# Kernel tuning notes

Hardware: AMD Instinct MI355X
Metric: run time of the kernel (lower is better)

The kernel has to match this reference:

```python
import jax, jax.numpy as jnp
import numpy as np

B, S, D_MODEL = 4, 2048, 1024
N_HEADS, D_HEAD = 16, 64
HIDDEN = N_HEADS * D_HEAD
N_PRIM, RANK = 16, 256
CHUNK = 64  # matches CHUNK_SIZE in the torch module


def setup_inputs() -> dict:
    key = jax.random.key(0)
    ks = jax.random.split(key, 16)
    def n(k, shape, scale=0.02):
        return jax.random.normal(k, shape, dtype=jnp.float32) * scale
    return {
        'x': jax.random.normal(ks[0], (B, S, D_MODEL), dtype=jnp.float32),
        'q_U': n(ks[1], (N_PRIM, D_MODEL, RANK)),
        'q_V': n(ks[2], (N_PRIM, RANK, HIDDEN)),
        'k_U': n(ks[3], (N_PRIM, D_MODEL, RANK)),
        'k_V': n(ks[4], (N_PRIM, RANK, HIDDEN)),
        'v_U': n(ks[5], (N_PRIM, D_MODEL, RANK)),
        'v_V': n(ks[6], (N_PRIM, RANK, HIDDEN)),
        'q_logits': jax.random.normal(ks[7], (N_PRIM,), dtype=jnp.float32),
        'k_logits': jax.random.normal(ks[8], (N_PRIM,), dtype=jnp.float32),
        'v_logits': jax.random.normal(ks[9], (N_PRIM,), dtype=jnp.float32),
        'gate_logits': jax.random.normal(ks[10], (N_PRIM,), dtype=jnp.float32),
        'decay_w': n(ks[11], (N_HEADS, D_MODEL), 0.03),
        'decay_b': jnp.full((N_HEADS,), -2.0, dtype=jnp.float32),
        'out_gate_w': n(ks[12], (HIDDEN, D_MODEL), 0.03),
        'out_proj_w': n(ks[13], (D_MODEL, HIDDEN), 0.03),
        'rms_w': jnp.ones((HIDDEN,), dtype=jnp.float32),
        'top_k': 4,
    }


def _bank_topk_fused(x, U, V, logits, top_k):
    """Top-k fused mixture of low-rank primitives: sum_j w_j * (x @ U_j @ V_j)."""
    w = jax.nn.softmax(logits)                      # [P]
    vals, idx = jax.lax.top_k(w, top_k)             # [k], [k]
    vals = vals / jnp.sum(vals)                     # renormalize selected weights
    Us = U[idx]                                     # [k, d_in, rank]
    Vs = V[idx]                                     # [k, rank, d_out]
    h = jnp.einsum('bsd,kdr->bskr', x, Us)          # low-rank bottleneck
    return jnp.einsum('bskr,kro,k->bso', h, Vs, vals)


def _chunked_scan(q, kv, log_decay):
    """Decay-gated linear recurrence via chunked parallel scan (CHUNK=64).
    q, kv: [B,S,H,D]; log_decay: [B,S,H,1]. Returns [B,S,H,D]."""
    b, s, h, d = q.shape
    nc = s // CHUNK
    # [NC, B, C, H, *] chunked layout for lax.scan over chunks
    qc = jnp.moveaxis(q.reshape(b, nc, CHUNK, h, d), 1, 0)
    kvc = jnp.moveaxis(kv.reshape(b, nc, CHUNK, h, d), 1, 0)
    ldc = jnp.moveaxis(log_decay.reshape(b, nc, CHUNK, h, 1), 1, 0)

    def step(state, inp):
        ld, kvs, qs = inp                            # [B,C,H,1], [B,C,H,D], [B,C,H,D]
        cum = jnp.cumsum(ld, axis=1)                 # cumulative log-decay in chunk
        last = cum[:, -1:]
        kv_shifted = kvs * jnp.exp(last - cum)
        new = jnp.exp(cum - last) * jnp.cumsum(kv_shifted, axis=1)
        chunk_states = state[:, None] * jnp.exp(cum) + new   # [B,C,H,D]
        out = qs * chunk_states
        return chunk_states[:, -1], out

    state0 = jnp.zeros((b, h, d), dtype=jnp.float32)
    _, outs = jax.lax.scan(step, state0, (ldc, kvc, qc))     # [NC,B,C,H,D]
    return jnp.moveaxis(outs, 0, 1).reshape(b, s, h, d)


def reference(x, q_U, q_V, k_U, k_V, v_U, v_V,
              q_logits, k_logits, v_logits, gate_logits,
              decay_w, decay_b, out_gate_w, out_proj_w, rms_w, top_k):
    b, s, _ = x.shape
    h, d = decay_w.shape[0], q_V.shape[-1] // decay_w.shape[0]

    q = _bank_topk_fused(x, q_U, q_V, q_logits, top_k).reshape(b, s, h, d)
    k = _bank_topk_fused(x, k_U, k_V, k_logits, top_k).reshape(b, s, h, d)
    v = _bank_topk_fused(x, v_U, v_V, v_logits, top_k).reshape(b, s, h, d)
    # gate shares the V bank (gate = v_bank.forward_topk_fused with gate weights)
    gate = _bank_topk_fused(x, v_U, v_V, gate_logits, top_k).reshape(b, s, h, d)

    log_decay = -jax.nn.softplus(jnp.einsum('bsd,hd->bsh', x, decay_w) + decay_b)[..., None]  # [B,S,H,1]
    kv = jax.nn.sigmoid(gate) * k * v

    out = _chunked_scan(q, kv.astype(jnp.float32), log_decay.astype(jnp.float32))
    out = out.reshape(b, s, h * d)

    # RMSNorm (torch default eps = finfo.eps for fp32)
    eps = jnp.finfo(jnp.float32).eps
    out = out * jax.lax.rsqrt(jnp.mean(out * out, axis=-1, keepdims=True) + eps) * rms_w
    out = out * jax.nn.sigmoid(jnp.einsum('bsd,od->bso', x, out_gate_w))
    return jnp.einsum('bsh,dh->bsd', out, out_proj_w)
```

## Files before the change

### kernel.cpp

```cpp
#include <hip/hip_runtime.h>
#include <hip/hip_bf16.h>

#define TOK 8192
#define SEQ 2048
#define CT  64
#define NC  32

typedef __attribute__((ext_vector_type(8))) short bf16x8;
typedef __attribute__((ext_vector_type(4))) float f32x4;
typedef unsigned short u16;
typedef unsigned int   u32;

__device__ __forceinline__ u16 f2bf(float f) {
    u32 u = __float_as_uint(f);
    u = (u + 0x7FFFu + ((u >> 16) & 1u)) >> 16;
    return (u16)u;
}
__device__ __forceinline__ float b2f(u16 h) { return __uint_as_float(((u32)h) << 16); }
__device__ __forceinline__ float sigf(float z) { return 1.f / (1.f + __expf(-z)); }

__device__ __forceinline__ void topk4(const float* __restrict__ lg, int* idx, float* wv)
{
    float v[16];
    #pragma unroll
    for (int i = 0; i < 16; i++) v[i] = lg[i];
    bool used[16];
    #pragma unroll
    for (int i = 0; i < 16; i++) used[i] = false;
    float val[4];
    #pragma unroll
    for (int k = 0; k < 4; k++) {
        int bi = 0; float bv = -3.0e38f;
        #pragma unroll
        for (int i = 0; i < 16; i++)
            if (!used[i] && v[i] > bv) { bv = v[i]; bi = i; }
        used[bi] = true; idx[k] = bi; val[k] = bv;
    }
    float e[4], s = 0.f;
    #pragma unroll
    for (int k = 0; k < 4; k++) { e[k] = expf(val[k] - val[0]); s += e[k]; }
    #pragma unroll
    for (int k = 0; k < 4; k++) wv[k] = e[k] / s;
}

__global__ __launch_bounds__(256)
void f2b_all(const float* __restrict__ x, const float* __restrict__ ogw,
             const float* __restrict__ opw,
             u16* __restrict__ xb, u16* __restrict__ ogwb, u16* __restrict__ opwb)
{
    const int i = blockIdx.x * 256 + threadIdx.x;
    const float* src; u16* dst; int off;
    if (i < 2097152)      { src = x;   dst = xb;   off = i; }
    else if (i < 2359296) { src = ogw; dst = ogwb; off = i - 2097152; }
    else                  { src = opw; dst = opwb; off = i - 2359296; }
    const float4 v = ((const float4*)src)[off];
    __align__(8) u16 t[4] = { f2bf(v.x), f2bf(v.y), f2bf(v.z), f2bf(v.w) };
    ((uint2*)dst)[off] = *(const uint2*)t;
}

__global__ __launch_bounds__(256)
void gather_all(const float* __restrict__ qU, const float* __restrict__ kU,
                const float* __restrict__ vU,
                const float* __restrict__ qV, const float* __restrict__ kV,
                const float* __restrict__ vV,
                const float* __restrict__ ql, const float* __restrict__ kl,
                const float* __restrict__ vl, const float* __restrict__ gl,
                u16* __restrict__ gU, u16* __restrict__ gVT)
{
    const int z = blockIdx.z;
    const int p = z & 3;
    const float* lg = (p == 0) ? ql : (p == 1) ? kl : (p == 2) ? vl : gl;
    int idx[4]; float wsel[4];
    topk4(lg, idx, wsel);
    const int tid = threadIdx.x;

    if (z < 4) {
        const float* V = (p == 0) ? qV : (p == 1) ? kV : vV;
        const int o0 = blockIdx.x * 64, k0 = blockIdx.y * 64;
        const int s = k0 >> 8, r0 = k0 & 255;
        const float* Vb = V + (size_t)idx[s] * (256 * 1024);
        __shared__ float tile[64][68];
        const int rr = tid >> 4, cc = (tid & 15) << 2;
        #pragma unroll
        for (int i = 0; i < 4; i++) {
            const float4 v = *(const float4*)(Vb + (size_t)(r0 + rr + 16 * i) * 1024 + o0 + cc);
            *(float4*)&tile[rr + 16 * i][cc] = v;
        }
        __syncthreads();
        const int oo = tid >> 4, kk = (tid & 15) << 2;
        u16* out = gVT + (size_t)p * 1048576;
        #pragma unroll
        for (int i = 0; i < 4; i++) {
            __align__(8) u16 t[4];
            #pragma unroll
            for (int j = 0; j < 4; j++) t[j] = f2bf(tile[kk + j][oo + 16 * i]);
            *(uint2*)(out + (size_t)(o0 + oo + 16 * i) * 1024 + k0 + kk) = *(const uint2*)t;
        }
    } else {
        const float* U = (p == 0) ? qU : (p == 1) ? kU : vU;
        const int d0 = blockIdx.x * 64, k0 = blockIdx.y * 64;
        const int s = k0 >> 8, r0 = k0 & 255;
        const float* Ub = U + (size_t)idx[s] * (1024 * 256);
        const float wq = wsel[s];
        u16* out = gU + (size_t)p * 1048576;
        const int rr = tid >> 4, cc = (tid & 15) << 2;
        #pragma unroll
        for (int i = 0; i < 4; i++) {
            const float4 v = *(const float4*)(Ub + (size_t)(d0 + rr + 16 * i) * 256 + r0 + cc);
            __align__(8) u16 t[4] = { f2bf(v.x * wq), f2bf(v.y * wq),
                                      f2bf(v.z * wq), f2bf(v.w * wq) };
            *(uint2*)(out + (size_t)(d0 + rr + 16 * i) * 1024 + k0 + cc) = *(const uint2*)t;
        }
    }
}

__global__ __launch_bounds__(256)
void mfma_gemm64(const u16* __restrict__ Asrc, const u16* __restrict__ Bsrc,
                 u16* __restrict__ Cout)
{
    __shared__ u16 As[64 * 64];
    __shared__ u16 Bs[64 * 64];
    const int z = blockIdx.z;
    const u16* A = Asrc + (size_t)z * 1048576;
    const u16* B = Bsrc + (size_t)z * 1048576;
    u16* C = Cout + (size_t)z * 1048576;
    const int tid = threadIdx.x, lane = tid & 63, wave = tid >> 6;
    const int m0 = blockIdx.y * 64, n0 = blockIdx.x * 64;
    const int wn = wave * 16;

    f32x4 acc[4];
    #pragma unroll
    for (int i = 0; i < 4; i++) acc[i] = (f32x4)0.f;

    for (int k0 = 0; k0 < 1024; k0 += 64) {
        __syncthreads();
        #pragma unroll
        for (int it = 0; it < 2; it++) {
            const int c   = it * 256 + tid;
            const int row = c >> 3, j = c & 7;
            const int g   = j ^ (row & 7);
            const u16* ga = A + (size_t)(m0 + row) * 1024 + k0 + g * 8;
            __builtin_amdgcn_global_load_lds(
                (const __attribute__((address_space(1))) u32*)ga,
                (__attribute__((address_space(3))) u32*)&As[(it * 256 + wave * 64) * 8],
                16, 0, 0);
            const u16* gb = B + (size_t)(n0 + row) * 1024 + k0 + g * 8;
            __builtin_amdgcn_global_load_lds(
                (const __attribute__((address_space(1))) u32*)gb,
                (__attribute__((address_space(3))) u32*)&Bs[(it * 256 + wave * 64) * 8],
                16, 0, 0);
        }
        __syncthreads();
        #pragma unroll
        for (int ks = 0; ks < 2; ks++) {
            const int gk = ks * 4 + (lane >> 4);
            const int rn = wn + (lane & 15);
            const int jb = gk ^ (rn & 7);
            const bf16x8 bfr = *(const bf16x8*)&Bs[rn * 64 + jb * 8];
            #pragma unroll
            for (int mi = 0; mi < 4; mi++) {
                const int rm = mi * 16 + (lane & 15);
                const int ja = gk ^ (rm & 7);
                const bf16x8 af = *(const bf16x8*)&As[rm * 64 + ja * 8];
                acc[mi] = __builtin_amdgcn_mfma_f32_16x16x32_bf16(af, bfr, acc[mi], 0, 0, 0);
            }
        }
    }
    const int col_l = lane & 15, row_l = (lane >> 4) * 4;
    #pragma unroll
    for (int mi = 0; mi < 4; mi++)
        #pragma unroll
        for (int i = 0; i < 4; i++)
            C[(size_t)(m0 + mi * 16 + row_l + i) * 1024 + n0 + wn + col_l] = f2bf(acc[mi][i]);
}

template<int OUTBF>
__global__ __launch_bounds__(256)
void mfma_gemm(const u16* __restrict__ Asrc, const u16* __restrict__ Bt,
               void* __restrict__ Cout, size_t astride, size_t bstride, size_t cstride)
{
    __shared__ u16 As[128 * 64];
    __shared__ u16 Bs[128 * 64];
    const int flat = blockIdx.x + 8 * (blockIdx.y + 64 * blockIdx.z);
    const int xcd = flat & 7;
    const int r   = flat >> 3;
    const int nb = r & 7, mlocal = (r >> 3) & 7, zb = r >> 6;
    const int m0 = (xcd * 8 + mlocal) * 128, n0 = nb * 128;

    const u16* A = Asrc + (size_t)zb * astride;
    const u16* B = Bt   + (size_t)zb * bstride;
    const int tid  = threadIdx.x;
    const int lane = tid & 63, wave = tid >> 6;
    const int wm = (wave >> 1) * 64, wn = (wave & 1) * 64;

    f32x4 acc[4][4];
    #pragma unroll
    for (int i = 0; i < 4; i++)
        #pragma unroll
        for (int j = 0; j < 4; j++) acc[i][j] = (f32x4)0.f;

    for (int k0 = 0; k0 < 1024; k0 += 64) {
        __syncthreads();
        #pragma unroll
        for (int it = 0; it < 4; it++) {
            const int c   = it * 256 + tid;
            const int row = c >> 3, j = c & 7;
            const int g   = j ^ (row & 7);
            const u16* ga = A + (size_t)(m0 + row) * 1024 + k0 + g * 8;
            __builtin_amdgcn_global_load_lds(
                (const __attribute__((address_space(1))) u32*)ga,
                (__attribute__((address_space(3))) u32*)&As[(it * 256 + wave * 64) * 8],
                16, 0, 0);
            const u16* gb = B + (size_t)(n0 + row) * 1024 + k0 + g * 8;
            __builtin_amdgcn_global_load_lds(
                (const __attribute__((address_space(1))) u32*)gb,
                (__attribute__((address_space(3))) u32*)&Bs[(it * 256 + wave * 64) * 8],
                16, 0, 0);
        }
        __syncthreads();
        #pragma unroll
        for (int ks = 0; ks < 2; ks++) {
            bf16x8 af[4], bfr[4];
            const int gk = ks * 4 + (lane >> 4);
            #pragma unroll
            for (int mi = 0; mi < 4; mi++) {
                const int rr  = wm + mi * 16 + (lane & 15);
                const int ja = gk ^ (rr & 7);
                af[mi] = *(const bf16x8*)&As[rr * 64 + ja * 8];
                const int rn = wn + mi * 16 + (lane & 15);
                const int jb = gk ^ (rn & 7);
                bfr[mi] = *(const bf16x8*)&Bs[rn * 64 + jb * 8];
            }
            #pragma unroll
            for (int mi = 0; mi < 4; mi++)
                #pragma unroll
                for (int ni = 0; ni < 4; ni++)
                    acc[mi][ni] = __builtin_amdgcn_mfma_f32_16x16x32_bf16(
                        af[mi], bfr[ni], acc[mi][ni], 0, 0, 0);
        }
    }
    const int col_l = lane & 15, row_l = (lane >> 4) * 4;
    if (OUTBF) {
        u16* C = (u16*)Cout + (size_t)zb * cstride;
        #pragma unroll
        for (int mi = 0; mi < 4; mi++)
            #pragma unroll
            for (int ni = 0; ni < 4; ni++)
                #pragma unroll
                for (int i = 0; i < 4; i++) {
                    const int rw  = m0 + wm + mi * 16 + row_l + i;
                    const int cn = n0 + wn + ni * 16 + col_l;
                    C[(size_t)rw * 1024 + cn] = f2bf(acc[mi][ni][i]);
                }
    } else {
        float* C = (float*)Cout + (size_t)zb * cstride;
        #pragma unroll
        for (int mi = 0; mi < 4; mi++)
            #pragma unroll
            for (int ni = 0; ni < 4; ni++)
                #pragma unroll
                for (int i = 0; i < 4; i++) {
                    const int rw  = m0 + wm + mi * 16 + row_l + i;
                    const int cn = n0 + wn + ni * 16 + col_l;
                    C[(size_t)rw * 1024 + cn] = acc[mi][ni][i];
                }
    }
}

__global__ __launch_bounds__(256)
void decay_kernel(const float* __restrict__ x, const float* __restrict__ dw,
                  const float* __restrict__ db, float* __restrict__ dec)
{
    const int wave = threadIdx.x >> 6, lane = threadIdx.x & 63;
    const int t = blockIdx.x * 4 + wave;
    const float4* x4 = (const float4*)(x + (size_t)t * 1024);
    float4 xv[4];
    #pragma unroll
    for (int i = 0; i < 4; i++) xv[i] = x4[lane + 64 * i];
    float p[16];
    #pragma unroll
    for (int h = 0; h < 16; h++) {
        const float4* w4 = (const float4*)(dw + (size_t)h * 1024);
        float s = 0.f;
        #pragma unroll
        for (int i = 0; i < 4; i++) {
            const float4 wv = w4[lane + 64 * i];
            s = fmaf(xv[i].x, wv.x, fmaf(xv[i].y, wv.y,
                fmaf(xv[i].z, wv.z, fmaf(xv[i].w, wv.w, s))));
        }
        p[h] = s;
    }
    #pragma unroll
    for (int off = 32; off > 0; off >>= 1)
        #pragma unroll
        for (int h = 0; h < 16; h++) p[h] += __shfl_xor(p[h], off);
    if (lane == 0) {
        #pragma unroll
        for (int h = 0; h < 16; h++)
            dec[(size_t)t * 16 + h] = 1.f / (1.f + __expf(p[h] + db[h]));
    }
}

__global__ __launch_bounds__(64)
void scan1(const u16* __restrict__ Kq, const u16* __restrict__ Vq, const u16* __restrict__ Gq,
           const float* __restrict__ dec, float* __restrict__ Lc, float* __restrict__ Pc)
{
    const int c = blockIdx.x & 31, h = (blockIdx.x >> 5) & 15, b = blockIdx.x >> 9;
    const int d = threadIdx.x;
    const size_t t0 = (size_t)b * SEQ + c * CT;
    const size_t base = t0 * 1024 + h * 64 + d;
    const u16* kp = Kq + base;
    const u16* vp = Vq + base;
    const u16* gp = Gq + base;
    const float* dp = dec + t0 * 16 + h;
    float s = 0.f, P = 1.f;
    #pragma unroll 4
    for (int t = 0; t < CT; t++) {
        const size_t o = (size_t)t * 1024;
        const float a  = dp[t * 16];
        const float kv = b2f(kp[o]) * b2f(vp[o]) * sigf(b2f(gp[o]));
        s = fmaf(a, s, kv);
        P *= a;
    }
    const int ci = (b * 16 + h) * NC + c;
    Lc[(size_t)ci * 64 + d] = s;
    if (d == 0) Pc[ci] = P;
}

__global__ __launch_bounds__(64)
void scan2(const float* __restrict__ Lc, const float* __restrict__ Pc, float* __restrict__ Ic)
{
    const int bh = blockIdx.x, d = threadIdx.x;
    float S = 0.f;
    for (int c = 0; c < NC; c++) {
        const int ci = bh * NC + c;
        Ic[(size_t)ci * 64 + d] = S;
        S = fmaf(Pc[ci], S, Lc[(size_t)ci * 64 + d]);
    }
}

__global__ __launch_bounds__(64)
void scan3(const u16* __restrict__ Qq, const u16* __restrict__ Kq,
           const u16* __restrict__ Vq, const u16* __restrict__ Gq,
           const float* __restrict__ dec, const float* __restrict__ Ic,
           u16* __restrict__ attb)
{
    const int c = blockIdx.x & 31, h = (blockIdx.x >> 5) & 15, b = blockIdx.x >> 9;
    const int d = threadIdx.x;
    const size_t t0 = (size_t)b * SEQ + c * CT;
    const size_t base = t0 * 1024 + h * 64 + d;
    const u16* qp = Qq + base;
    const u16* kp = Kq + base;
    const u16* vp = Vq + base;
    const u16* gp = Gq + base;
    const float* dp = dec + t0 * 16 + h;
    const int ci = (b * 16 + h) * NC + c;
    float s = Ic[(size_t)ci * 64 + d];
    #pragma unroll 4
    for (int t = 0; t < CT; t++) {
        const size_t o = (size_t)t * 1024;
        const float a  = dp[t * 16];
        const float kv = b2f(kp[o]) * b2f(vp[o]) * sigf(b2f(gp[o]));
        s = fmaf(a, s, kv);
        attb[base + o] = f2bf(b2f(qp[o]) * s);
    }
}

__global__ __launch_bounds__(256)
void rms_gate(const u16* __restrict__ attb, const u16* __restrict__ gpre,
              const float* __restrict__ rmsw, u16* __restrict__ o)
{
    const size_t t = blockIdx.x;
    const int tid = threadIdx.x;
    const ushort4 a4 = ((const ushort4*)(attb + t * 1024))[tid];
    const float ax = b2f(a4.x), ay = b2f(a4.y), az = b2f(a4.z), aw = b2f(a4.w);
    float ss = ax*ax + ay*ay + az*az + aw*aw;
    #pragma unroll
    for (int d = 32; d > 0; d >>= 1) ss += __shfl_down(ss, d);
    __shared__ float red[4];
    if ((tid & 63) == 0) red[tid >> 6] = ss;
    __syncthreads();
    const float tot = red[0] + red[1] + red[2] + red[3];
    const float scale = rsqrtf(tot * (1.0f / 1024.0f) + 1.1920929e-7f);
    const ushort4 g4 = ((const ushort4*)(gpre + t * 1024))[tid];
    const float4 w   = ((const float4*)rmsw)[tid];
    __align__(8) u16 r[4];
    r[0] = f2bf(ax * scale * w.x * sigf(b2f(g4.x)));
    r[1] = f2bf(ay * scale * w.y * sigf(b2f(g4.y)));
    r[2] = f2bf(az * scale * w.z * sigf(b2f(g4.z)));
    r[3] = f2bf(aw * scale * w.w * sigf(b2f(g4.w)));
    ((uint2*)(o + t * 1024))[tid] = *(const uint2*)r;
}

extern "C" void kernel_launch(void* const* d_in, const int* in_sizes, int n_in,
                              void* d_out, int out_size, void* d_ws, size_t ws_size,
                              hipStream_t stream)
{
    const float* x    = (const float*)d_in[0];
    const float* qU   = (const float*)d_in[1];
    const float* qV   = (const float*)d_in[2];
    const float* kU   = (const float*)d_in[3];
    const float* kV   = (const float*)d_in[4];
    const float* vU   = (const float*)d_in[5];
    const float* vV   = (const float*)d_in[6];
    const float* ql   = (const float*)d_in[7];
    const float* kl   = (const float*)d_in[8];
    const float* vl   = (const float*)d_in[9];
    const float* gl   = (const float*)d_in[10];
    const float* dw   = (const float*)d_in[11];
    const float* db   = (const float*)d_in[12];
    const float* ogw  = (const float*)d_in[13];
    const float* opw  = (const float*)d_in[14];
    const float* rmsw = (const float*)d_in[15];

    char* w = (char*)d_ws;
    float* dec  = (float*)(w + 0);
    u16*   WT   = (u16*)  (w + 524288);
    u16*   xb   = (u16*)  (w + 11010048);
    u16*   opwb = (u16*)  (w + 27787264);
    u16*   QKVG = (u16*)  (w + 29884416);
    u16*   RMSO = (u16*)  (w + 113770496);
    u16*   ATTb = (u16*)  (w + 130547712);
    float* Lc   = (float*)(w + 147324928);
    float* Ic   = (float*)(w + 147849216);
    float* Pc   = (float*)(w + 148373504);
    u16*   gU   = QKVG;
    u16*   gVT  = QKVG + 4194304;
    u16*   ogwb = WT + 4 * 1048576;
    u16*   GPRE = QKVG + 4 * 8388608;

    f2b_all<<<10240, 256, 0, stream>>>(x, ogw, opw, xb, ogwb, opwb);

    gather_all<<<dim3(16, 16, 8), 256, 0, stream>>>(qU, kU, vU, qV, kV, vV,
                                                    ql, kl, vl, gl, gU, gVT);

    mfma_gemm64<<<dim3(16, 16, 4), 256, 0, stream>>>(gVT, gU, WT);

    mfma_gemm<1><<<dim3(8, 64, 5), 256, 0, stream>>>(xb, WT, QKVG,
                                                     (size_t)0, (size_t)1048576,
                                                     (size_t)8388608);

    decay_kernel<<<2048, 256, 0, stream>>>(x, dw, db, dec);

    scan1<<<2048, 64, 0, stream>>>(QKVG + 8388608, QKVG + 16777216, QKVG + 25165824,
                                   dec, Lc, Pc);
    scan2<<<64, 64, 0, stream>>>(Lc, Pc, Ic);
    scan3<<<2048, 64, 0, stream>>>(QKVG, QKVG + 8388608, QKVG + 16777216, QKVG + 25165824,
                                   dec, Ic, ATTb);

    rms_gate<<<8192, 256, 0, stream>>>(ATTb, GPRE, rmsw, RMSO);

    mfma_gemm<0><<<dim3(8, 64, 1), 256, 0, stream>>>(RMSO, opwb, (float*)d_out, 0, 0, 0);
}
```

Baseline: 411.7 us.

## Merge prep kernels, halve scan chunk size, and fold inter-chunk scan into scan3

```diff
diff --git a/kernel.cpp b/kernel.cpp
--- a/kernel.cpp
+++ b/kernel.cpp
@@ -3,8 +3,8 @@
 
 #define TOK 8192
 #define SEQ 2048
-#define CT  64
-#define NC  32
+#define CT  32
+#define NC  64
 
 typedef __attribute__((ext_vector_type(8))) short bf16x8;
 typedef __attribute__((ext_vector_type(4))) float f32x4;
@@ -44,72 +44,110 @@
 }
 
 __global__ __launch_bounds__(256)
-void f2b_all(const float* __restrict__ x, const float* __restrict__ ogw,
-             const float* __restrict__ opw,
-             u16* __restrict__ xb, u16* __restrict__ ogwb, u16* __restrict__ opwb)
-{
-    const int i = blockIdx.x * 256 + threadIdx.x;
-    const float* src; u16* dst; int off;
-    if (i < 2097152)      { src = x;   dst = xb;   off = i; }
-    else if (i < 2359296) { src = ogw; dst = ogwb; off = i - 2097152; }
-    else                  { src = opw; dst = opwb; off = i - 2359296; }
-    const float4 v = ((const float4*)src)[off];
-    __align__(8) u16 t[4] = { f2bf(v.x), f2bf(v.y), f2bf(v.z), f2bf(v.w) };
-    ((uint2*)dst)[off] = *(const uint2*)t;
-}
-
-__global__ __launch_bounds__(256)
-void gather_all(const float* __restrict__ qU, const float* __restrict__ kU,
-                const float* __restrict__ vU,
-                const float* __restrict__ qV, const float* __restrict__ kV,
-                const float* __restrict__ vV,
-                const float* __restrict__ ql, const float* __restrict__ kl,
-                const float* __restrict__ vl, const float* __restrict__ gl,
-                u16* __restrict__ gU, u16* __restrict__ gVT)
-{
-    const int z = blockIdx.z;
-    const int p = z & 3;
-    const float* lg = (p == 0) ? ql : (p == 1) ? kl : (p == 2) ? vl : gl;
-    int idx[4]; float wsel[4];
-    topk4(lg, idx, wsel);
+void prep(const float* __restrict__ x, const float* __restrict__ ogw,
+          const float* __restrict__ opw,
+          const float* __restrict__ qU, const float* __restrict__ kU,
+          const float* __restrict__ vU,
+          const float* __restrict__ qV, const float* __restrict__ kV,
+          const float* __restrict__ vV,
+          const float* __restrict__ ql, const float* __restrict__ kl,
+          const float* __restrict__ vl, const float* __restrict__ gl,
+          const float* __restrict__ dw, const float* __restrict__ db,
+          u16* __restrict__ xb, u16* __restrict__ ogwb, u16* __restrict__ opwb,
+          u16* __restrict__ gU, u16* __restrict__ gVT, float* __restrict__ dec)
+{
+    const int blk = blockIdx.x;
     const int tid = threadIdx.x;
 
-    if (z < 4) {
-        const float* V = (p == 0) ? qV : (p == 1) ? kV : vV;
-        const int o0 = blockIdx.x * 64, k0 = blockIdx.y * 64;
-        const int s = k0 >> 8, r0 = k0 & 255;
-        const float* Vb = V + (size_t)idx[s] * (256 * 1024);
-        __shared__ float tile[64][68];
-        const int rr = tid >> 4, cc = (tid & 15) << 2;
-        #pragma unroll
-        for (int i = 0; i < 4; i++) {
-            const float4 v = *(const float4*)(Vb + (size_t)(r0 + rr + 16 * i) * 1024 + o0 + cc);
-            *(float4*)&tile[rr + 16 * i][cc] = v;
-        }
-        __syncthreads();
-        const int oo = tid >> 4, kk = (tid & 15) << 2;
-        u16* out = gVT + (size_t)p * 1048576;
-        #pragma unroll
-        for (int i = 0; i < 4; i++) {
-            __align__(8) u16 t[4];
-            #pragma unroll
-            for (int j = 0; j < 4; j++) t[j] = f2bf(tile[kk + j][oo + 16 * i]);
-            *(uint2*)(out + (size_t)(o0 + oo + 16 * i) * 1024 + k0 + kk) = *(const uint2*)t;
-        }
-    } else {
-        const float* U = (p == 0) ? qU : (p == 1) ? kU : vU;
-        const int d0 = blockIdx.x * 64, k0 = blockIdx.y * 64;
-        const int s = k0 >> 8, r0 = k0 & 255;
-        const float* Ub = U + (size_t)idx[s] * (1024 * 256);
-        const float wq = wsel[s];
-        u16* out = gU + (size_t)p * 1048576;
-        const int rr = tid >> 4, cc = (tid & 15) << 2;
-        #pragma unroll
-        for (int i = 0; i < 4; i++) {
-            const float4 v = *(const float4*)(Ub + (size_t)(d0 + rr + 16 * i) * 256 + r0 + cc);
-            __align__(8) u16 t[4] = { f2bf(v.x * wq), f2bf(v.y * wq),
-                                      f2bf(v.z * wq), f2bf(v.w * wq) };
-            *(uint2*)(out + (size_t)(d0 + rr + 16 * i) * 1024 + k0 + cc) = *(const uint2*)t;
+    if (blk < 10240) {
+        const int i = blk * 256 + tid;
+        const float* src; u16* dst; int off;
+        if (i < 2097152)      { src = x;   dst = xb;   off = i; }
+        else if (i < 2359296) { src = ogw; dst = ogwb; off = i - 2097152; }
+        else                  { src = opw; dst = opwb; off = i - 2359296; }
+        const float4 v = ((const float4*)src)[off];
+        __align__(8) u16 t[4] = { f2bf(v.x), f2bf(v.y), f2bf(v.z), f2bf(v.w) };
+        ((uint2*)dst)[off] = *(const uint2*)t;
+        return;
+    }
+    if (blk < 12288) {
+        const int local = blk - 10240;
+        const int z = local >> 8;
+        const int bx = local & 15, by = (local >> 4) & 15;
+        const int p = z & 3;
+        const float* lg = (p == 0) ? ql : (p == 1) ? kl : (p == 2) ? vl : gl;
+        int idx[4]; float wsel[4];
+        topk4(lg, idx, wsel);
+
+        if (z < 4) {
+            const float* V = (p == 0) ? qV : (p == 1) ? kV : vV;
+            const int o0 = bx * 64, k0 = by * 64;
+            const int s = k0 >> 8, r0 = k0 & 255;
+            const float* Vb = V + (size_t)idx[s] * (256 * 1024);
+            __shared__ float tile[64][68];
+            const int rr = tid >> 4, cc = (tid & 15) << 2;
+            #pragma unroll
+            for (int i = 0; i < 4; i++) {
+                const float4 v = *(const float4*)(Vb + (size_t)(r0 + rr + 16 * i) * 1024 + o0 + cc);
+                *(float4*)&tile[rr + 16 * i][cc] = v;
+            }
+            __syncthreads();
+            const int oo = tid >> 4, kk = (tid & 15) << 2;
+            u16* out = gVT + (size_t)p * 1048576;
+            #pragma unroll
+            for (int i = 0; i < 4; i++) {
+                __align__(8) u16 t[4];
+                #pragma unroll
+                for (int j = 0; j < 4; j++) t[j] = f2bf(tile[kk + j][oo + 16 * i]);
+                *(uint2*)(out + (size_t)(o0 + oo + 16 * i) * 1024 + k0 + kk) = *(const uint2*)t;
+            }
+        } else {
+            const float* U = (p == 0) ? qU : (p == 1) ? kU : vU;
+            const int d0 = bx * 64, k0 = by * 64;
+            const int s = k0 >> 8, r0 = k0 & 255;
+            const float* Ub = U + (size_t)idx[s] * (1024 * 256);
+            const float wq = wsel[s];
+            u16* out = gU + (size_t)p * 1048576;
+            const int rr = tid >> 4, cc = (tid & 15) << 2;
+            #pragma unroll
+            for (int i = 0; i < 4; i++) {
+                const float4 v = *(const float4*)(Ub + (size_t)(d0 + rr + 16 * i) * 256 + r0 + cc);
+                __align__(8) u16 t[4] = { f2bf(v.x * wq), f2bf(v.y * wq),
+                                          f2bf(v.z * wq), f2bf(v.w * wq) };
+                *(uint2*)(out + (size_t)(d0 + rr + 16 * i) * 1024 + k0 + cc) = *(const uint2*)t;
+            }
+        }
+        return;
+    }
+    {
+        const int tg = blk - 12288;
+        const int wave = tid >> 6, lane = tid & 63;
+        const int t = tg * 4 + wave;
+        const float4* x4 = (const float4*)(x + (size_t)t * 1024);
+        float4 xv[4];
+        #pragma unroll
+        for (int i = 0; i < 4; i++) xv[i] = x4[lane + 64 * i];
+        float p[16];
+        #pragma unroll
+        for (int h = 0; h < 16; h++) {
+            const float4* w4 = (const float4*)(dw + (size_t)h * 1024);
+            float s = 0.f;
+            #pragma unroll
+            for (int i = 0; i < 4; i++) {
+                const float4 wv = w4[lane + 64 * i];
+                s = fmaf(xv[i].x, wv.x, fmaf(xv[i].y, wv.y,
+                    fmaf(xv[i].z, wv.z, fmaf(xv[i].w, wv.w, s))));
+            }
+            p[h] = s;
+        }
+        #pragma unroll
+        for (int off = 32; off > 0; off >>= 1)
+            #pragma unroll
+            for (int h = 0; h < 16; h++) p[h] += __shfl_xor(p[h], off);
+        if (lane == 0) {
+            #pragma unroll
+            for (int h = 0; h < 16; h++)
+                dec[(size_t)t * 16 + h] = 1.f / (1.f + __expf(p[h] + db[h]));
         }
     }
 }
@@ -267,45 +305,12 @@
     }
 }
 
-__global__ __launch_bounds__(256)
-void decay_kernel(const float* __restrict__ x, const float* __restrict__ dw,
-                  const float* __restrict__ db, float* __restrict__ dec)
-{
-    const int wave = threadIdx.x >> 6, lane = threadIdx.x & 63;
-    const int t = blockIdx.x * 4 + wave;
-    const float4* x4 = (const float4*)(x + (size_t)t * 1024);
-    float4 xv[4];
-    #pragma unroll
-    for (int i = 0; i < 4; i++) xv[i] = x4[lane + 64 * i];
-    float p[16];
-    #pragma unroll
-    for (int h = 0; h < 16; h++) {
-        const float4* w4 = (const float4*)(dw + (size_t)h * 1024);
-        float s = 0.f;
-        #pragma unroll
-        for (int i = 0; i < 4; i++) {
-            const float4 wv = w4[lane + 64 * i];
-            s = fmaf(xv[i].x, wv.x, fmaf(xv[i].y, wv.y,
-                fmaf(xv[i].z, wv.z, fmaf(xv[i].w, wv.w, s))));
-        }
-        p[h] = s;
-    }
-    #pragma unroll
-    for (int off = 32; off > 0; off >>= 1)
-        #pragma unroll
-        for (int h = 0; h < 16; h++) p[h] += __shfl_xor(p[h], off);
-    if (lane == 0) {
-        #pragma unroll
-        for (int h = 0; h < 16; h++)
-            dec[(size_t)t * 16 + h] = 1.f / (1.f + __expf(p[h] + db[h]));
-    }
-}
-
 __global__ __launch_bounds__(64)
 void scan1(const u16* __restrict__ Kq, const u16* __restrict__ Vq, const u16* __restrict__ Gq,
-           const float* __restrict__ dec, float* __restrict__ Lc, float* __restrict__ Pc)
-{
-    const int c = blockIdx.x & 31, h = (blockIdx.x >> 5) & 15, b = blockIdx.x >> 9;
+           const float* __restrict__ dec, u16* __restrict__ kvb,
+           float* __restrict__ Lc, float* __restrict__ Pc)
+{
+    const int c = blockIdx.x & (NC - 1), h = (blockIdx.x >> 6) & 15, b = blockIdx.x >> 10;
     const int d = threadIdx.x;
     const size_t t0 = (size_t)b * SEQ + c * CT;
     const size_t base = t0 * 1024 + h * 64 + d;
@@ -318,8 +323,9 @@
     for (int t = 0; t < CT; t++) {
         const size_t o = (size_t)t * 1024;
         const float a  = dp[t * 16];
-        const float kv = b2f(kp[o]) * b2f(vp[o]) * sigf(b2f(gp[o]));
-        s = fmaf(a, s, kv);
+        const u16 kq = f2bf(b2f(kp[o]) * b2f(vp[o]) * sigf(b2f(gp[o])));
+        kvb[base + o] = kq;
+        s = fmaf(a, s, b2f(kq));
         P *= a;
     }
     const int ci = (b * 16 + h) * NC + c;
@@ -328,40 +334,29 @@
 }
 
 __global__ __launch_bounds__(64)
-void scan2(const float* __restrict__ Lc, const float* __restrict__ Pc, float* __restrict__ Ic)
-{
-    const int bh = blockIdx.x, d = threadIdx.x;
-    float S = 0.f;
-    for (int c = 0; c < NC; c++) {
-        const int ci = bh * NC + c;
-        Ic[(size_t)ci * 64 + d] = S;
-        S = fmaf(Pc[ci], S, Lc[(size_t)ci * 64 + d]);
-    }
-}
-
-__global__ __launch_bounds__(64)
-void scan3(const u16* __restrict__ Qq, const u16* __restrict__ Kq,
-           const u16* __restrict__ Vq, const u16* __restrict__ Gq,
-           const float* __restrict__ dec, const float* __restrict__ Ic,
+void scan3(const u16* __restrict__ Qq, const u16* __restrict__ kvb,
+           const float* __restrict__ dec,
+           const float* __restrict__ Lc, const float* __restrict__ Pc,
            u16* __restrict__ attb)
 {
-    const int c = blockIdx.x & 31, h = (blockIdx.x >> 5) & 15, b = blockIdx.x >> 9;
+    const int c = blockIdx.x & (NC - 1), h = (blockIdx.x >> 6) & 15, b = blockIdx.x >> 10;
     const int d = threadIdx.x;
     const size_t t0 = (size_t)b * SEQ + c * CT;
     const size_t base = t0 * 1024 + h * 64 + d;
     const u16* qp = Qq + base;
-    const u16* kp = Kq + base;
-    const u16* vp = Vq + base;
-    const u16* gp = Gq + base;
+    const u16* kp = kvb + base;
     const float* dp = dec + t0 * 16 + h;
-    const int ci = (b * 16 + h) * NC + c;
-    float s = Ic[(size_t)ci * 64 + d];
+
+    const int ci0 = (b * 16 + h) * NC;
+    float s = 0.f;
+    for (int cc = 0; cc < c; cc++)
+        s = fmaf(Pc[ci0 + cc], s, Lc[(size_t)(ci0 + cc) * 64 + d]);
+
     #pragma unroll 4
     for (int t = 0; t < CT; t++) {
         const size_t o = (size_t)t * 1024;
         const float a  = dp[t * 16];
-        const float kv = b2f(kp[o]) * b2f(vp[o]) * sigf(b2f(gp[o]));
-        s = fmaf(a, s, kv);
+        s = fmaf(a, s, b2f(kp[o]));
         attb[base + o] = f2bf(b2f(qp[o]) * s);
     }
 }
@@ -421,18 +416,17 @@
     u16*   QKVG = (u16*)  (w + 29884416);
     u16*   RMSO = (u16*)  (w + 113770496);
     u16*   ATTb = (u16*)  (w + 130547712);
-    float* Lc   = (float*)(w + 147324928);
-    float* Ic   = (float*)(w + 147849216);
-    float* Pc   = (float*)(w + 148373504);
+    u16*   kvb  = (u16*)  (w + 147324928);
+    float* Lc   = (float*)(w + 164102144);
+    float* Pc   = (float*)(w + 165150720);
     u16*   gU   = QKVG;
     u16*   gVT  = QKVG + 4194304;
     u16*   ogwb = WT + 4 * 1048576;
     u16*   GPRE = QKVG + 4 * 8388608;
 
-    f2b_all<<<10240, 256, 0, stream>>>(x, ogw, opw, xb, ogwb, opwb);
-
-    gather_all<<<dim3(16, 16, 8), 256, 0, stream>>>(qU, kU, vU, qV, kV, vV,
-                                                    ql, kl, vl, gl, gU, gVT);
+    prep<<<14336, 256, 0, stream>>>(x, ogw, opw, qU, kU, vU, qV, kV, vV,
+                                    ql, kl, vl, gl, dw, db,
+                                    xb, ogwb, opwb, gU, gVT, dec);
 
     mfma_gemm64<<<dim3(16, 16, 4), 256, 0, stream>>>(gVT, gU, WT);
 
@@ -440,13 +434,9 @@
                                                      (size_t)0, (size_t)1048576,
                                                      (size_t)8388608);
 
-    decay_kernel<<<2048, 256, 0, stream>>>(x, dw, db, dec);
-
-    scan1<<<2048, 64, 0, stream>>>(QKVG + 8388608, QKVG + 16777216, QKVG + 25165824,
-                                   dec, Lc, Pc);
-    scan2<<<64, 64, 0, stream>>>(Lc, Pc, Ic);
-    scan3<<<2048, 64, 0, stream>>>(QKVG, QKVG + 8388608, QKVG + 16777216, QKVG + 25165824,
-                                   dec, Ic, ATTb);
+    scan1<<<4096, 64, 0, stream>>>(QKVG + 8388608, QKVG + 16777216, QKVG + 25165824,
+                                   dec, kvb, Lc, Pc);
+    scan3<<<4096, 64, 0, stream>>>(QKVG, kvb, dec, Lc, Pc, ATTb);
 
     rms_gate<<<8192, 256, 0, stream>>>(ATTb, GPRE, rmsw, RMSO);
 
```

Measured after the change: 397.8 us. 3.4% less time.
